# Performance work log

Measured on AMD Instinct MI355X. Metric: run time of the kernel, lower is better.

## Reference

```python
import jax, jax.numpy as jnp
import numpy as np

B, I, H = 8192, 1024, 1024

def setup_inputs() -> dict:
    key = jax.random.key(0)
    ks = jax.random.split(key, 5)
    return {
        "x": jax.random.normal(ks[0], (B, I), dtype=jnp.float32),
        "m_prev": jax.random.normal(ks[1], (B, H), dtype=jnp.float32),
        "c_prev": jax.random.normal(ks[2], (B, H), dtype=jnp.float32),
        "w_m": jax.random.normal(ks[3], (H, 8 * H), dtype=jnp.float32),
        "w_inputs": jax.random.normal(ks[4], (I, 8 * H), dtype=jnp.float32),
    }

def reference(x, m_prev, c_prev, w_m, w_inputs):
    hidden = w_m.shape[0]
    m_mat = m_prev @ w_m              # [B, 8H]
    in_mat = x @ w_inputs             # [B, 8H]
    # 8-way split along feature dim
    ms = jnp.split(m_mat, 8, axis=1)
    xs = jnp.split(in_mat, 8, axis=1)
    sig, th, rl = jax.nn.sigmoid, jnp.tanh, jax.nn.relu
    l1_0 = sig(xs[0] + ms[0])
    l1_1 = rl(xs[1] + ms[1])
    l1_2 = sig(xs[2] + ms[2])
    l1_3 = rl(xs[3] * ms[3])
    l1_4 = th(xs[4] + ms[4])
    l1_5 = sig(xs[5] + ms[5])
    l1_6 = th(xs[6] + ms[6])
    l1_7 = sig(xs[7] + ms[7])
    l2_0 = th(l1_0 * l1_1)
    l2_1 = th(l1_2 + l1_3)
    l2_2 = th(l1_4 * l1_5)
    l2_3 = sig(l1_6 + l1_7)
    l2_0 = th(l2_0 + c_prev)
    new_c = l2_0 * l2_1
    l3_1 = th(l2_2 + l2_3)
    new_m = th(new_c * l3_1)
    return (new_m, new_c)
```

## Files before the change

kernel.cpp:

```cpp
#include <hip/hip_runtime.h>
#include <stdint.h>
#include <stddef.h>


typedef _Float16 half8 __attribute__((ext_vector_type(8)));
typedef float f32x4 __attribute__((ext_vector_type(4)));
typedef float float4v __attribute__((ext_vector_type(4)));
typedef unsigned int u32;
typedef u32 u32x4 __attribute__((ext_vector_type(4)));

__device__ __forceinline__ float fsig(float x) { return 1.0f / (1.0f + __expf(-x)); }
__device__ __forceinline__ float ftanh(float x) { return 2.0f * fsig(2.0f * x) - 1.0f; }
__device__ __forceinline__ u32 packh(_Float16 a, _Float16 b) {
  union { u32 u; _Float16 h[2]; } p;
  p.h[0] = a; p.h[1] = b; return p.u;
}

__device__ __forceinline__ void gload16(const void* g, void* l) {
  __builtin_amdgcn_global_load_lds(
      (const __attribute__((address_space(1))) void*)g,
      (__attribute__((address_space(3))) void*)l, 16, 0, 0);
}

__global__ __launch_bounds__(256) void prep_b(
    const float* __restrict__ w_inputs, const float* __restrict__ w_m,
    u32* __restrict__ wsB) {
  const int kt = blockIdx.x;
  const int hblk = blockIdx.y;
  const int tid = threadIdx.x;
  const int n = tid & 15;
  const int g = (tid >> 4) & 7;
  const int mat = tid >> 7;
  const float* w = mat ? w_m : w_inputs;
  const float* src = w + (size_t)kt * 32 * 8192 + (size_t)g * 1024 + hblk * 16 + n;
  const int kx4 = ((n >> 1) & 3) << 2;
  u32 hw[16], lw[16];
#pragma unroll
  for (int k2 = 0; k2 < 16; ++k2) {
    const float v0 = src[(size_t)(2 * k2) * 8192];
    const float v1 = src[(size_t)(2 * k2 + 1) * 8192];
    const _Float16 h0 = (_Float16)v0, h1 = (_Float16)v1;
    hw[k2 ^ kx4] = packh(h0, h1);
    lw[k2 ^ kx4] = packh((_Float16)(v0 - (float)h0), (_Float16)(v1 - (float)h1));
  }
  u32* dhi = wsB + ((size_t)kt * 64 + hblk) * 8192 + mat * 2048 + g * 256 + n * 16;
  u32* dlo = dhi + 4096;
#pragma unroll
  for (int t4 = 0; t4 < 4; ++t4) {
    u32x4 a = {hw[t4 * 4], hw[t4 * 4 + 1], hw[t4 * 4 + 2], hw[t4 * 4 + 3]};
    *(u32x4*)(dhi + t4 * 4) = a;
    u32x4 b = {lw[t4 * 4], lw[t4 * 4 + 1], lw[t4 * 4 + 2], lw[t4 * 4 + 3]};
    *(u32x4*)(dlo + t4 * 4) = b;
  }
}

__global__ __launch_bounds__(256) void split_a(
    const float4v* __restrict__ in, half8* __restrict__ hi, half8* __restrict__ lo) {
  const size_t idx = (size_t)blockIdx.x * 256 + threadIdx.x;
  const float4v a = in[idx * 2];
  const float4v b = in[idx * 2 + 1];
  half8 h, l;
#pragma unroll
  for (int j = 0; j < 4; ++j) {
    const float v = a[j]; const _Float16 hv = (_Float16)v;
    h[j] = hv; l[j] = (_Float16)(v - (float)hv);
  }
#pragma unroll
  for (int j = 0; j < 4; ++j) {
    const float v = b[j]; const _Float16 hv = (_Float16)v;
    h[4 + j] = hv; l[4 + j] = (_Float16)(v - (float)hv);
  }
  hi[idx] = h; lo[idx] = l;
}

__global__ __launch_bounds__(256, 2) void nascell_fast(
    const _Float16* __restrict__ xh_g, const _Float16* __restrict__ xl_g,
    const _Float16* __restrict__ mh_g, const _Float16* __restrict__ ml_g,
    const u32* __restrict__ wsB,
    const float* __restrict__ c_prev,
    float* __restrict__ out) {
  __shared__ short lds[32768];
  const int tid = threadIdx.x;
  const int wid = tid >> 6;
  const int lane = tid & 63;
  const int row0 = blockIdx.y * 256;
  const int hblk = blockIdx.x;
  const int m16 = lane & 15;
  const int q = lane >> 4;
  const int qsw = (q ^ ((m16 >> 1) & 3)) * 8;

  const size_t arow = (size_t)(row0 + wid * 64 + m16);
  const _Float16* xhb = xh_g + arow * 1024 + q * 8;
  const _Float16* xlb = xl_g + arow * 1024 + q * 8;
  const _Float16* mhb = mh_g + arow * 1024 + q * 8;
  const _Float16* mlb = ml_g + arow * 1024 + q * 8;

  const char* wsb = (const char*)wsB + (size_t)hblk * 32768 + wid * 8192 + lane * 16;
  char* ldsb0 = (char*)lds + wid * 8192;

  f32x4 acc[4][9];
#pragma unroll
  for (int r = 0; r < 4; ++r)
#pragma unroll
    for (int gg = 0; gg < 9; ++gg) acc[r][gg] = (f32x4)0.0f;

#pragma unroll
  for (int i = 0; i < 8; ++i) gload16(wsb + i * 1024, ldsb0 + i * 1024);

  for (int kt = 0; kt < 32; ++kt) {
    __syncthreads();

    half8 axh[4], axl[4], amh[4], aml[4];
#pragma unroll
    for (int r = 0; r < 4; ++r) {
      axh[r] = *(const half8*)(xhb + (size_t)r * 16384 + kt * 32);
      axl[r] = *(const half8*)(xlb + (size_t)r * 16384 + kt * 32);
      amh[r] = *(const half8*)(mhb + (size_t)r * 16384 + kt * 32);
      aml[r] = *(const half8*)(mlb + (size_t)r * 16384 + kt * 32);
    }
    __builtin_amdgcn_sched_barrier(0);
    if (kt < 31) {
      const char* src = wsb + (size_t)(kt + 1) * 2097152;
      char* dst = (char*)lds + ((kt + 1) & 1) * 32768 + wid * 8192;
#pragma unroll
      for (int i = 0; i < 8; ++i) gload16(src + i * 1024, dst + i * 1024);
    }
    __builtin_amdgcn_sched_barrier(0);

    const short* bb = lds + (kt & 1) * 16384;

#pragma unroll
    for (int c = 0; c < 8; ++c) {
      const int bo = c * 512 + m16 * 32 + qsw;
      const half8 bxh = *(const half8*)(bb + bo);
      const half8 bxl = *(const half8*)(bb + 8192 + bo);
#pragma unroll
      for (int r = 0; r < 4; ++r) {
        f32x4 t = acc[r][c];
        t = __builtin_amdgcn_mfma_f32_16x16x32_f16(axh[r], bxh, t, 0, 0, 0);
        t = __builtin_amdgcn_mfma_f32_16x16x32_f16(axh[r], bxl, t, 0, 0, 0);
        t = __builtin_amdgcn_mfma_f32_16x16x32_f16(axl[r], bxh, t, 0, 0, 0);
        acc[r][c] = t;
      }
    }

#pragma unroll
    for (int c = 0; c < 8; ++c) {
      const int bo = 4096 + c * 512 + m16 * 32 + qsw;
      const half8 bmh = *(const half8*)(bb + bo);
      const half8 bml = *(const half8*)(bb + 8192 + bo);
      const int tgt = (c == 3) ? 8 : c;
#pragma unroll
      for (int r = 0; r < 4; ++r) {
        f32x4 t = acc[r][tgt];
        t = __builtin_amdgcn_mfma_f32_16x16x32_f16(amh[r], bmh, t, 0, 0, 0);
        t = __builtin_amdgcn_mfma_f32_16x16x32_f16(amh[r], bml, t, 0, 0, 0);
        t = __builtin_amdgcn_mfma_f32_16x16x32_f16(aml[r], bmh, t, 0, 0, 0);
        acc[r][tgt] = t;
      }
    }
  }

  float* out_m = out;
  float* out_c = out + (size_t)8192 * 1024;
  const int h = hblk * 16 + m16;
#pragma unroll
  for (int r = 0; r < 4; ++r) {
#pragma unroll
    for (int i = 0; i < 4; ++i) {
      const int grow = row0 + wid * 64 + r * 16 + q * 4 + i;
      const float p0 = acc[r][0][i], p1 = acc[r][1][i], p2 = acc[r][2][i];
      const float x3 = acc[r][3][i], p4 = acc[r][4][i], p5 = acc[r][5][i];
      const float p6 = acc[r][6][i], p7 = acc[r][7][i], m3 = acc[r][8][i];
      const float cp = c_prev[(size_t)grow * 1024 + h];
      float l1_0 = fsig(p0);
      float l1_1 = fmaxf(p1, 0.0f);
      float l1_2 = fsig(p2);
      float l1_3 = fmaxf(x3 * m3, 0.0f);
      float l1_4 = ftanh(p4);
      float l1_5 = fsig(p5);
      float l1_6 = ftanh(p6);
      float l1_7 = fsig(p7);
      float l2_0 = ftanh(l1_0 * l1_1);
      float l2_1 = ftanh(l1_2 + l1_3);
      float l2_2 = ftanh(l1_4 * l1_5);
      float l2_3 = fsig(l1_6 + l1_7);
      float l2_0b = ftanh(l2_0 + cp);
      float nc = l2_0b * l2_1;
      float l3_1 = ftanh(l2_2 + l2_3);
      float nm = ftanh(nc * l3_1);
      out_m[(size_t)grow * 1024 + h] = nm;
      out_c[(size_t)grow * 1024 + h] = nc;
    }
  }
}

__global__ __launch_bounds__(256, 2) void nascell_main(
    const float* __restrict__ x,
    const float* __restrict__ m_prev,
    const float* __restrict__ c_prev,
    const float* __restrict__ w_inputs,
    const float* __restrict__ w_m,
    float* __restrict__ out) {
  __shared__ short lds[17408];
  const int tid = threadIdx.x;
  const int wid = tid >> 6;
  const int lane = tid & 63;
  const int row0 = blockIdx.y * 256;
  const int h0 = blockIdx.x * 16;
  const int m16 = lane & 15;
  const int q = lane >> 4;

  const int bmat = tid >> 7;
  const int bg = (tid >> 4) & 7;
  const int bkp = (tid & 15) * 2;
  const float* wsrc = bmat ? w_m : w_inputs;
  const float* wrow_base = wsrc + (size_t)bkp * 8192 + (size_t)bg * 1024 + (size_t)h0;
  short* bh = lds + bmat * 4352 + bg * 544 + (bkp ^ ((bg & 3) << 3));
  short* bl = bh + 8704;

  const float* axp[4];
  const float* amp[4];
#pragma unroll
  for (int r = 0; r < 4; ++r) {
    const size_t arow = (size_t)(row0 + wid * 64 + r * 16 + m16);
    axp[r] = x + arow * 1024 + q * 8;
    amp[r] = m_prev + arow * 1024 + q * 8;
  }

  f32x4 acc[4][9];
#pragma unroll
  for (int r = 0; r < 4; ++r)
#pragma unroll
    for (int gg = 0; gg < 9; ++gg) acc[r][gg] = (f32x4)0.0f;

  for (int kt = 0; kt < 32; ++kt) {
    const float* wr = wrow_base + (size_t)kt * 32 * 8192;
    float4v b0 = *(const float4v*)(wr);
    float4v b1 = *(const float4v*)(wr + 4);
    float4v b2 = *(const float4v*)(wr + 8);
    float4v b3 = *(const float4v*)(wr + 12);
    float4v d0 = *(const float4v*)(wr + 8192);
    float4v d1 = *(const float4v*)(wr + 8196);
    float4v d2 = *(const float4v*)(wr + 8200);
    float4v d3 = *(const float4v*)(wr + 8204);

    float4v xa[4][2];
#pragma unroll
    for (int r = 0; r < 4; ++r) {
      xa[r][0] = *(const float4v*)(axp[r] + kt * 32);
      xa[r][1] = *(const float4v*)(axp[r] + kt * 32 + 4);
    }

    __syncthreads();

#pragma unroll
    for (int n = 0; n < 16; ++n) {
      const float r0 = (n < 4 ? b0[n & 3] : n < 8 ? b1[n & 3] : n < 12 ? b2[n & 3] : b3[n & 3]);
      const float r1 = (n < 4 ? d0[n & 3] : n < 8 ? d1[n & 3] : n < 12 ? d2[n & 3] : d3[n & 3]);
      const _Float16 h0v = (_Float16)r0;
      const _Float16 h1v = (_Float16)r1;
      *(u32*)(bh + n * 32) = packh(h0v, h1v);
      const _Float16 l0v = (_Float16)(r0 - (float)h0v);
      const _Float16 l1v = (_Float16)(r1 - (float)h1v);
      *(u32*)(bl + n * 32) = packh(l0v, l1v);
    }

    half8 axh[4], axl[4];
#pragma unroll
    for (int r = 0; r < 4; ++r)
#pragma unroll
      for (int j = 0; j < 8; ++j) {
        const float v = xa[r][j >> 2][j & 3];
        const _Float16 hv = (_Float16)v;
        axh[r][j] = hv;
        axl[r][j] = (_Float16)(v - (float)hv);
      }

    __syncthreads();

    float4v ma[4][2];
#pragma unroll
    for (int r = 0; r < 4; ++r) {
      ma[r][0] = *(const float4v*)(amp[r] + kt * 32);
      ma[r][1] = *(const float4v*)(amp[r] + kt * 32 + 4);
    }

#pragma unroll
    for (int c = 0; c < 8; ++c) {
      const int qs = (q ^ (c & 3)) * 8;
      const int bo = c * 544 + m16 * 32 + qs;
      half8 bxh = *(const half8*)(lds + bo);
      half8 bxl = *(const half8*)(lds + 8704 + bo);
#pragma unroll
      for (int r = 0; r < 4; ++r) {
        f32x4 t = acc[r][c];
        t = __builtin_amdgcn_mfma_f32_16x16x32_f16(axh[r], bxh, t, 0, 0, 0);
        t = __builtin_amdgcn_mfma_f32_16x16x32_f16(axh[r], bxl, t, 0, 0, 0);
        t = __builtin_amdgcn_mfma_f32_16x16x32_f16(axl[r], bxh, t, 0, 0, 0);
        acc[r][c] = t;
      }
    }

    half8 amh[4], aml[4];
#pragma unroll
    for (int r = 0; r < 4; ++r)
#pragma unroll
      for (int j = 0; j < 8; ++j) {
        const float v = ma[r][j >> 2][j & 3];
        const _Float16 hv = (_Float16)v;
        amh[r][j] = hv;
        aml[r][j] = (_Float16)(v - (float)hv);
      }

#pragma unroll
    for (int c = 0; c < 8; ++c) {
      const int qs = (q ^ (c & 3)) * 8;
      const int bo = 4352 + c * 544 + m16 * 32 + qs;
      half8 bmh = *(const half8*)(lds + bo);
      half8 bml = *(const half8*)(lds + 8704 + bo);
      const int tgt = (c == 3) ? 8 : c;
#pragma unroll
      for (int r = 0; r < 4; ++r) {
        f32x4 t = acc[r][tgt];
        t = __builtin_amdgcn_mfma_f32_16x16x32_f16(amh[r], bmh, t, 0, 0, 0);
        t = __builtin_amdgcn_mfma_f32_16x16x32_f16(amh[r], bml, t, 0, 0, 0);
        t = __builtin_amdgcn_mfma_f32_16x16x32_f16(aml[r], bmh, t, 0, 0, 0);
        acc[r][tgt] = t;
      }
    }
  }

  float* out_m = out;
  float* out_c = out + (size_t)8192 * 1024;
  const int h = h0 + m16;
#pragma unroll
  for (int r = 0; r < 4; ++r) {
#pragma unroll
    for (int i = 0; i < 4; ++i) {
      const int grow = row0 + wid * 64 + r * 16 + q * 4 + i;
      const float p0 = acc[r][0][i], p1 = acc[r][1][i], p2 = acc[r][2][i];
      const float x3 = acc[r][3][i], p4 = acc[r][4][i], p5 = acc[r][5][i];
      const float p6 = acc[r][6][i], p7 = acc[r][7][i], m3 = acc[r][8][i];
      const float cp = c_prev[(size_t)grow * 1024 + h];
      float l1_0 = fsig(p0);
      float l1_1 = fmaxf(p1, 0.0f);
      float l1_2 = fsig(p2);
      float l1_3 = fmaxf(x3 * m3, 0.0f);
      float l1_4 = ftanh(p4);
      float l1_5 = fsig(p5);
      float l1_6 = ftanh(p6);
      float l1_7 = fsig(p7);
      float l2_0 = ftanh(l1_0 * l1_1);
      float l2_1 = ftanh(l1_2 + l1_3);
      float l2_2 = ftanh(l1_4 * l1_5);
      float l2_3 = fsig(l1_6 + l1_7);
      float l2_0b = ftanh(l2_0 + cp);
      float nc = l2_0b * l2_1;
      float l3_1 = ftanh(l2_2 + l2_3);
      float nm = ftanh(nc * l3_1);
      out_m[(size_t)grow * 1024 + h] = nm;
      out_c[(size_t)grow * 1024 + h] = nc;
    }
  }
}

extern "C" void kernel_launch(void* const* d_in, const int* in_sizes, int n_in,
                              void* d_out, int out_size, void* d_ws, size_t ws_size,
                              hipStream_t stream) {
  (void)in_sizes; (void)n_in; (void)out_size;
  const float* x        = (const float*)d_in[0];
  const float* m_prev   = (const float*)d_in[1];
  const float* c_prev   = (const float*)d_in[2];
  const float* w_m      = (const float*)d_in[3];
  const float* w_inputs = (const float*)d_in[4];
  float* out = (float*)d_out;

  if (ws_size >= 134217728ull && d_ws != nullptr) {
    u32* wsB = (u32*)d_ws;
    _Float16* xh = (_Float16*)((char*)d_ws + 67108864);
    _Float16* xl = xh + 8388608;
    _Float16* mh = xl + 8388608;
    _Float16* ml = mh + 8388608;
    prep_b<<<dim3(32, 64), 256, 0, stream>>>(w_inputs, w_m, wsB);
    split_a<<<4096, 256, 0, stream>>>((const float4v*)x, (half8*)xh, (half8*)xl);
    split_a<<<4096, 256, 0, stream>>>((const float4v*)m_prev, (half8*)mh, (half8*)ml);
    nascell_fast<<<dim3(64, 32), 256, 0, stream>>>(xh, xl, mh, ml, wsB, c_prev, out);
  } else {
    dim3 grid(64, 32);
    nascell_main<<<grid, 256, 0, stream>>>(x, m_prev, c_prev, w_inputs, w_m, out);
  }
}
```

Baseline: 873.0 us.

## Read B fragments directly from global in MFMA layout, drop LDS staging

The weight prep kernel now writes hi/lo fp16 tiles laid out so each lane can load its MFMA B fragment with one contiguous 16-byte global load. The main kernel drops the LDS double buffer, global_load_lds prefetch and per-iteration __syncthreads, and reads B straight from global/L2. The two activation split launches are merged into one launch. This removes barrier and LDS traffic but loses the explicit prefetch overlap, and all four waves in a block now read the same B tile from cache.

```diff
diff --git a/kernel.cpp b/kernel.cpp
--- a/kernel.cpp
+++ b/kernel.cpp
@@ -16,15 +16,9 @@
   p.h[0] = a; p.h[1] = b; return p.u;
 }
 
-__device__ __forceinline__ void gload16(const void* g, void* l) {
-  __builtin_amdgcn_global_load_lds(
-      (const __attribute__((address_space(1))) void*)g,
-      (__attribute__((address_space(3))) void*)l, 16, 0, 0);
-}
-
 __global__ __launch_bounds__(256) void prep_b(
     const float* __restrict__ w_inputs, const float* __restrict__ w_m,
-    u32* __restrict__ wsB) {
+    char* __restrict__ wsB) {
   const int kt = blockIdx.x;
   const int hblk = blockIdx.y;
   const int tid = threadIdx.x;
@@ -33,29 +27,36 @@
   const int mat = tid >> 7;
   const float* w = mat ? w_m : w_inputs;
   const float* src = w + (size_t)kt * 32 * 8192 + (size_t)g * 1024 + hblk * 16 + n;
-  const int kx4 = ((n >> 1) & 3) << 2;
-  u32 hw[16], lw[16];
-#pragma unroll
-  for (int k2 = 0; k2 < 16; ++k2) {
-    const float v0 = src[(size_t)(2 * k2) * 8192];
-    const float v1 = src[(size_t)(2 * k2 + 1) * 8192];
-    const _Float16 h0 = (_Float16)v0, h1 = (_Float16)v1;
-    hw[k2 ^ kx4] = packh(h0, h1);
-    lw[k2 ^ kx4] = packh((_Float16)(v0 - (float)h0), (_Float16)(v1 - (float)h1));
-  }
-  u32* dhi = wsB + ((size_t)kt * 64 + hblk) * 8192 + mat * 2048 + g * 256 + n * 16;
-  u32* dlo = dhi + 4096;
-#pragma unroll
-  for (int t4 = 0; t4 < 4; ++t4) {
-    u32x4 a = {hw[t4 * 4], hw[t4 * 4 + 1], hw[t4 * 4 + 2], hw[t4 * 4 + 3]};
-    *(u32x4*)(dhi + t4 * 4) = a;
-    u32x4 b = {lw[t4 * 4], lw[t4 * 4 + 1], lw[t4 * 4 + 2], lw[t4 * 4 + 3]};
-    *(u32x4*)(dlo + t4 * 4) = b;
-  }
-}
-
-__global__ __launch_bounds__(256) void split_a(
-    const float4v* __restrict__ in, half8* __restrict__ hi, half8* __restrict__ lo) {
+  _Float16 hs[32], ls[32];
+#pragma unroll
+  for (int k = 0; k < 32; ++k) {
+    const float v = src[(size_t)k * 8192];
+    const _Float16 h = (_Float16)v;
+    hs[k] = h;
+    ls[k] = (_Float16)(v - (float)h);
+  }
+  char* tile = wsB + ((size_t)hblk * 32 + kt) * 32768;
+  char* hi = tile + (size_t)((mat * 8 + g) * 2 + 0) * 1024;
+  char* lo = hi + 1024;
+#pragma unroll
+  for (int kc = 0; kc < 4; ++kc) {
+    u32x4 a = {packh(hs[kc * 8 + 0], hs[kc * 8 + 1]), packh(hs[kc * 8 + 2], hs[kc * 8 + 3]),
+               packh(hs[kc * 8 + 4], hs[kc * 8 + 5]), packh(hs[kc * 8 + 6], hs[kc * 8 + 7])};
+    *(u32x4*)(hi + (kc * 16 + n) * 16) = a;
+    u32x4 b = {packh(ls[kc * 8 + 0], ls[kc * 8 + 1]), packh(ls[kc * 8 + 2], ls[kc * 8 + 3]),
+               packh(ls[kc * 8 + 4], ls[kc * 8 + 5]), packh(ls[kc * 8 + 6], ls[kc * 8 + 7])};
+    *(u32x4*)(lo + (kc * 16 + n) * 16) = b;
+  }
+}
+
+__global__ __launch_bounds__(256) void split_ab(
+    const float4v* __restrict__ xin, const float4v* __restrict__ min,
+    half8* __restrict__ xhi, half8* __restrict__ xlo,
+    half8* __restrict__ mhi, half8* __restrict__ mlo) {
+  const int which = blockIdx.y;
+  const float4v* in = which ? min : xin;
+  half8* hi = which ? mhi : xhi;
+  half8* lo = which ? mlo : xlo;
   const size_t idx = (size_t)blockIdx.x * 256 + threadIdx.x;
   const float4v a = in[idx * 2];
   const float4v b = in[idx * 2 + 1];
@@ -73,13 +74,12 @@
   hi[idx] = h; lo[idx] = l;
 }
 
-__global__ __launch_bounds__(256, 2) void nascell_fast(
+__global__ __launch_bounds__(256, 2) void nascell_v3(
     const _Float16* __restrict__ xh_g, const _Float16* __restrict__ xl_g,
     const _Float16* __restrict__ mh_g, const _Float16* __restrict__ ml_g,
-    const u32* __restrict__ wsB,
+    const char* __restrict__ wsB,
     const float* __restrict__ c_prev,
     float* __restrict__ out) {
-  __shared__ short lds[32768];
   const int tid = threadIdx.x;
   const int wid = tid >> 6;
   const int lane = tid & 63;
@@ -87,7 +87,6 @@
   const int hblk = blockIdx.x;
   const int m16 = lane & 15;
   const int q = lane >> 4;
-  const int qsw = (q ^ ((m16 >> 1) & 3)) * 8;
 
   const size_t arow = (size_t)(row0 + wid * 64 + m16);
   const _Float16* xhb = xh_g + arow * 1024 + q * 8;
@@ -95,8 +94,7 @@
   const _Float16* mhb = mh_g + arow * 1024 + q * 8;
   const _Float16* mlb = ml_g + arow * 1024 + q * 8;
 
-  const char* wsb = (const char*)wsB + (size_t)hblk * 32768 + wid * 8192 + lane * 16;
-  char* ldsb0 = (char*)lds + wid * 8192;
+  const char* bt = wsB + (size_t)hblk * 32 * 32768 + lane * 16;
 
   f32x4 acc[4][9];
 #pragma unroll
@@ -104,11 +102,9 @@
 #pragma unroll
     for (int gg = 0; gg < 9; ++gg) acc[r][gg] = (f32x4)0.0f;
 
-#pragma unroll
-  for (int i = 0; i < 8; ++i) gload16(wsb + i * 1024, ldsb0 + i * 1024);
-
+#pragma unroll 1
   for (int kt = 0; kt < 32; ++kt) {
-    __syncthreads();
+    const char* tb = bt + (size_t)kt * 32768;
 
     half8 axh[4], axl[4], amh[4], aml[4];
 #pragma unroll
@@ -118,22 +114,11 @@
       amh[r] = *(const half8*)(mhb + (size_t)r * 16384 + kt * 32);
       aml[r] = *(const half8*)(mlb + (size_t)r * 16384 + kt * 32);
     }
-    __builtin_amdgcn_sched_barrier(0);
-    if (kt < 31) {
-      const char* src = wsb + (size_t)(kt + 1) * 2097152;
-      char* dst = (char*)lds + ((kt + 1) & 1) * 32768 + wid * 8192;
-#pragma unroll
-      for (int i = 0; i < 8; ++i) gload16(src + i * 1024, dst + i * 1024);
-    }
-    __builtin_amdgcn_sched_barrier(0);
-
-    const short* bb = lds + (kt & 1) * 16384;
 
 #pragma unroll
     for (int c = 0; c < 8; ++c) {
-      const int bo = c * 512 + m16 * 32 + qsw;
-      const half8 bxh = *(const half8*)(bb + bo);
-      const half8 bxl = *(const half8*)(bb + 8192 + bo);
+      const half8 bxh = *(const half8*)(tb + (size_t)(c * 2) * 1024);
+      const half8 bxl = *(const half8*)(tb + (size_t)(c * 2 + 1) * 1024);
 #pragma unroll
       for (int r = 0; r < 4; ++r) {
         f32x4 t = acc[r][c];
@@ -146,9 +131,8 @@
 
 #pragma unroll
     for (int c = 0; c < 8; ++c) {
-      const int bo = 4096 + c * 512 + m16 * 32 + qsw;
-      const half8 bmh = *(const half8*)(bb + bo);
-      const half8 bml = *(const half8*)(bb + 8192 + bo);
+      const half8 bmh = *(const half8*)(tb + 16384 + (size_t)(c * 2) * 1024);
+      const half8 bml = *(const half8*)(tb + 16384 + (size_t)(c * 2 + 1) * 1024);
       const int tgt = (c == 3) ? 8 : c;
 #pragma unroll
       for (int r = 0; r < 4; ++r) {
@@ -377,15 +361,16 @@
   float* out = (float*)d_out;
 
   if (ws_size >= 134217728ull && d_ws != nullptr) {
-    u32* wsB = (u32*)d_ws;
+    char* wsB = (char*)d_ws;
     _Float16* xh = (_Float16*)((char*)d_ws + 67108864);
     _Float16* xl = xh + 8388608;
     _Float16* mh = xl + 8388608;
     _Float16* ml = mh + 8388608;
     prep_b<<<dim3(32, 64), 256, 0, stream>>>(w_inputs, w_m, wsB);
-    split_a<<<4096, 256, 0, stream>>>((const float4v*)x, (half8*)xh, (half8*)xl);
-    split_a<<<4096, 256, 0, stream>>>((const float4v*)m_prev, (half8*)mh, (half8*)ml);
-    nascell_fast<<<dim3(64, 32), 256, 0, stream>>>(xh, xl, mh, ml, wsB, c_prev, out);
+    split_ab<<<dim3(4096, 2), 256, 0, stream>>>(
+        (const float4v*)x, (const float4v*)m_prev,
+        (half8*)xh, (half8*)xl, (half8*)mh, (half8*)ml);
+    nascell_v3<<<dim3(64, 32), 256, 0, stream>>>(xh, xl, mh, ml, wsB, c_prev, out);
   } else {
     dim3 grid(64, 32);
     nascell_main<<<grid, 256, 0, stream>>>(x, m_prev, c_prev, w_inputs, w_m, out);
```

Measured after the change: 1.053 ms. 20.6% more time.

## Merge prep kernels and deepen GEMM pipeline to four LDS stages

Applied to the files above, without the earlier changes.

Merges the weight-repacking and activation-splitting kernels into one launch and moves the weight workspace to an hblk-major layout so each block reads contiguous chunks. The main GEMM loop now splits each k-tile into separate x and m half-stages across four 16KB LDS slots. It waits on explicit vmcnt counts with raw s_barrier instead of __syncthreads, and uses setprio around the MFMA passes. The goal is to keep more loads in flight and overlap global-to-LDS copies with MFMA work, at the cost of fragile hand-managed waitcnt accounting.

```diff
diff --git a/kernel.cpp b/kernel.cpp
--- a/kernel.cpp
+++ b/kernel.cpp
@@ -22,64 +22,146 @@
       (__attribute__((address_space(3))) void*)l, 16, 0, 0);
 }
 
-__global__ __launch_bounds__(256) void prep_b(
+__global__ __launch_bounds__(256) void prep_all(
     const float* __restrict__ w_inputs, const float* __restrict__ w_m,
-    u32* __restrict__ wsB) {
-  const int kt = blockIdx.x;
-  const int hblk = blockIdx.y;
+    const float4v* __restrict__ xin, const float4v* __restrict__ min,
+    u32* __restrict__ wsB,
+    half8* __restrict__ xhi, half8* __restrict__ xlo,
+    half8* __restrict__ mhi, half8* __restrict__ mlo) {
+  const int bid = blockIdx.x;
   const int tid = threadIdx.x;
-  const int n = tid & 15;
-  const int g = (tid >> 4) & 7;
-  const int mat = tid >> 7;
-  const float* w = mat ? w_m : w_inputs;
-  const float* src = w + (size_t)kt * 32 * 8192 + (size_t)g * 1024 + hblk * 16 + n;
-  const int kx4 = ((n >> 1) & 3) << 2;
-  u32 hw[16], lw[16];
-#pragma unroll
-  for (int k2 = 0; k2 < 16; ++k2) {
-    const float v0 = src[(size_t)(2 * k2) * 8192];
-    const float v1 = src[(size_t)(2 * k2 + 1) * 8192];
-    const _Float16 h0 = (_Float16)v0, h1 = (_Float16)v1;
-    hw[k2 ^ kx4] = packh(h0, h1);
-    lw[k2 ^ kx4] = packh((_Float16)(v0 - (float)h0), (_Float16)(v1 - (float)h1));
-  }
-  u32* dhi = wsB + ((size_t)kt * 64 + hblk) * 8192 + mat * 2048 + g * 256 + n * 16;
-  u32* dlo = dhi + 4096;
-#pragma unroll
-  for (int t4 = 0; t4 < 4; ++t4) {
-    u32x4 a = {hw[t4 * 4], hw[t4 * 4 + 1], hw[t4 * 4 + 2], hw[t4 * 4 + 3]};
-    *(u32x4*)(dhi + t4 * 4) = a;
-    u32x4 b = {lw[t4 * 4], lw[t4 * 4 + 1], lw[t4 * 4 + 2], lw[t4 * 4 + 3]};
-    *(u32x4*)(dlo + t4 * 4) = b;
-  }
-}
-
-__global__ __launch_bounds__(256) void split_a(
-    const float4v* __restrict__ in, half8* __restrict__ hi, half8* __restrict__ lo) {
-  const size_t idx = (size_t)blockIdx.x * 256 + threadIdx.x;
-  const float4v a = in[idx * 2];
-  const float4v b = in[idx * 2 + 1];
-  half8 h, l;
-#pragma unroll
-  for (int j = 0; j < 4; ++j) {
-    const float v = a[j]; const _Float16 hv = (_Float16)v;
-    h[j] = hv; l[j] = (_Float16)(v - (float)hv);
-  }
-#pragma unroll
-  for (int j = 0; j < 4; ++j) {
-    const float v = b[j]; const _Float16 hv = (_Float16)v;
-    h[4 + j] = hv; l[4 + j] = (_Float16)(v - (float)hv);
-  }
-  hi[idx] = h; lo[idx] = l;
-}
-
-__global__ __launch_bounds__(256, 2) void nascell_fast(
+  if (bid < 2048) {
+    const int kt = bid & 31;
+    const int hblk = bid >> 5;
+    const int n = tid & 15;
+    const int g = (tid >> 4) & 7;
+    const int mat = tid >> 7;
+    const float* w = mat ? w_m : w_inputs;
+    const float* src = w + (size_t)kt * 32 * 8192 + (size_t)g * 1024 + hblk * 16 + n;
+    const int kx4 = ((n >> 1) & 3) << 2;
+    u32 hw[16], lw[16];
+#pragma unroll
+    for (int k2 = 0; k2 < 16; ++k2) {
+      const float v0 = src[(size_t)(2 * k2) * 8192];
+      const float v1 = src[(size_t)(2 * k2 + 1) * 8192];
+      const _Float16 h0 = (_Float16)v0, h1 = (_Float16)v1;
+      hw[k2 ^ kx4] = packh(h0, h1);
+      lw[k2 ^ kx4] = packh((_Float16)(v0 - (float)h0), (_Float16)(v1 - (float)h1));
+    }
+    u32* dhi = wsB + ((size_t)(hblk * 32 + kt) * 2 + mat) * 4096 + g * 256 + n * 16;
+    u32* dlo = dhi + 2048;
+#pragma unroll
+    for (int t4 = 0; t4 < 4; ++t4) {
+      u32x4 a = {hw[t4 * 4], hw[t4 * 4 + 1], hw[t4 * 4 + 2], hw[t4 * 4 + 3]};
+      *(u32x4*)(dhi + t4 * 4) = a;
+      u32x4 b = {lw[t4 * 4], lw[t4 * 4 + 1], lw[t4 * 4 + 2], lw[t4 * 4 + 3]};
+      *(u32x4*)(dlo + t4 * 4) = b;
+    }
+  } else {
+    const int sid = bid - 2048;
+    const int which = sid >> 12;
+    const int bx = sid & 4095;
+    const float4v* in = which ? min : xin;
+    half8* hi = which ? mhi : xhi;
+    half8* lo = which ? mlo : xlo;
+    const size_t idx = (size_t)bx * 256 + tid;
+    const float4v a = in[idx * 2];
+    const float4v b = in[idx * 2 + 1];
+    half8 h, l;
+#pragma unroll
+    for (int j = 0; j < 4; ++j) {
+      const float v = a[j]; const _Float16 hv = (_Float16)v;
+      h[j] = hv; l[j] = (_Float16)(v - (float)hv);
+    }
+#pragma unroll
+    for (int j = 0; j < 4; ++j) {
+      const float v = b[j]; const _Float16 hv = (_Float16)v;
+      h[4 + j] = hv; l[4 + j] = (_Float16)(v - (float)hv);
+    }
+    hi[idx] = h; lo[idx] = l;
+  }
+}
+
+
+#define NAS_WAITBAR(Wlit)                                                  \
+  do {                                                                     \
+    asm volatile("s_waitcnt vmcnt(" #Wlit ")" ::: "memory");               \
+    __builtin_amdgcn_s_barrier();                                          \
+    __builtin_amdgcn_sched_barrier(0);                                     \
+  } while (0)
+
+#define NAS_STAGE(KT, MAT, SLOT)                                           \
+  do {                                                                     \
+    const char* s_ = wsb + (size_t)(((KT) * 2 + (MAT)) * 16384);           \
+    char* d_ = ldsb + (SLOT) * 16384;                                      \
+    gload16(s_, d_);                                                       \
+    gload16(s_ + 4096, d_ + 4096);                                         \
+    gload16(s_ + 8192, d_ + 8192);                                         \
+    gload16(s_ + 12288, d_ + 12288);                                       \
+  } while (0)
+
+#define NAS_LOADX(KT)                                                      \
+  do {                                                                     \
+    _Pragma("unroll") for (int r_ = 0; r_ < 4; ++r_) {                     \
+      axh[r_] = *(const half8*)(xhb + r_ * 16384 + (KT) * 32);             \
+      axl[r_] = *(const half8*)(xlb + r_ * 16384 + (KT) * 32);             \
+    }                                                                      \
+  } while (0)
+
+#define NAS_LOADM(KT)                                                      \
+  do {                                                                     \
+    _Pragma("unroll") for (int r_ = 0; r_ < 4; ++r_) {                     \
+      amh[r_] = *(const half8*)(mhb + r_ * 16384 + (KT) * 32);             \
+      aml[r_] = *(const half8*)(mlb + r_ * 16384 + (KT) * 32);             \
+    }                                                                      \
+  } while (0)
+
+#define NAS_XPASS(SLOT)                                                    \
+  do {                                                                     \
+    const short* bb_ = lds_s + (SLOT) * 8192;                              \
+    __builtin_amdgcn_s_setprio(1);                                         \
+    _Pragma("unroll") for (int c_ = 0; c_ < 8; ++c_) {                     \
+      const int bo_ = c_ * 512 + m16 * 32 + qsw;                           \
+      const half8 bh_ = *(const half8*)(bb_ + bo_);                        \
+      const half8 bl_ = *(const half8*)(bb_ + 4096 + bo_);                 \
+      _Pragma("unroll") for (int r_ = 0; r_ < 4; ++r_) {                   \
+        f32x4 t_ = acc[r_][c_];                                            \
+        t_ = __builtin_amdgcn_mfma_f32_16x16x32_f16(axh[r_], bh_, t_, 0, 0, 0); \
+        t_ = __builtin_amdgcn_mfma_f32_16x16x32_f16(axh[r_], bl_, t_, 0, 0, 0); \
+        t_ = __builtin_amdgcn_mfma_f32_16x16x32_f16(axl[r_], bh_, t_, 0, 0, 0); \
+        acc[r_][c_] = t_;                                                  \
+      }                                                                    \
+    }                                                                      \
+    __builtin_amdgcn_s_setprio(0);                                         \
+  } while (0)
+
+#define NAS_MPASS(SLOT)                                                    \
+  do {                                                                     \
+    const short* bb_ = lds_s + (SLOT) * 8192;                              \
+    __builtin_amdgcn_s_setprio(1);                                         \
+    _Pragma("unroll") for (int c_ = 0; c_ < 8; ++c_) {                     \
+      const int bo_ = c_ * 512 + m16 * 32 + qsw;                           \
+      const half8 bh_ = *(const half8*)(bb_ + bo_);                        \
+      const half8 bl_ = *(const half8*)(bb_ + 4096 + bo_);                 \
+      const int tgt_ = (c_ == 3) ? 8 : c_;                                 \
+      _Pragma("unroll") for (int r_ = 0; r_ < 4; ++r_) {                   \
+        f32x4 t_ = acc[r_][tgt_];                                          \
+        t_ = __builtin_amdgcn_mfma_f32_16x16x32_f16(amh[r_], bh_, t_, 0, 0, 0); \
+        t_ = __builtin_amdgcn_mfma_f32_16x16x32_f16(amh[r_], bl_, t_, 0, 0, 0); \
+        t_ = __builtin_amdgcn_mfma_f32_16x16x32_f16(aml[r_], bh_, t_, 0, 0, 0); \
+        acc[r_][tgt_] = t_;                                                \
+      }                                                                    \
+    }                                                                      \
+    __builtin_amdgcn_s_setprio(0);                                         \
+  } while (0)
+
+__global__ __launch_bounds__(256, 2) void nascell_v6(
     const _Float16* __restrict__ xh_g, const _Float16* __restrict__ xl_g,
     const _Float16* __restrict__ mh_g, const _Float16* __restrict__ ml_g,
-    const u32* __restrict__ wsB,
+    const char* __restrict__ wsB,
     const float* __restrict__ c_prev,
     float* __restrict__ out) {
-  __shared__ short lds[32768];
+  __shared__ short lds_s[32768];
   const int tid = threadIdx.x;
   const int wid = tid >> 6;
   const int lane = tid & 63;
@@ -89,14 +171,13 @@
   const int q = lane >> 4;
   const int qsw = (q ^ ((m16 >> 1) & 3)) * 8;
 
-  const size_t arow = (size_t)(row0 + wid * 64 + m16);
-  const _Float16* xhb = xh_g + arow * 1024 + q * 8;
-  const _Float16* xlb = xl_g + arow * 1024 + q * 8;
-  const _Float16* mhb = mh_g + arow * 1024 + q * 8;
-  const _Float16* mlb = ml_g + arow * 1024 + q * 8;
-
-  const char* wsb = (const char*)wsB + (size_t)hblk * 32768 + wid * 8192 + lane * 16;
-  char* ldsb0 = (char*)lds + wid * 8192;
+  const _Float16* xhb = xh_g + (size_t)(row0 + wid * 64 + m16) * 1024 + q * 8;
+  const _Float16* xlb = xl_g + (size_t)(row0 + wid * 64 + m16) * 1024 + q * 8;
+  const _Float16* mhb = mh_g + (size_t)(row0 + wid * 64 + m16) * 1024 + q * 8;
+  const _Float16* mlb = ml_g + (size_t)(row0 + wid * 64 + m16) * 1024 + q * 8;
+
+  const char* wsb = wsB + (size_t)hblk * 1048576 + tid * 16;
+  char* ldsb = (char*)lds_s + tid * 16;
 
   f32x4 acc[4][9];
 #pragma unroll
@@ -104,62 +185,26 @@
 #pragma unroll
     for (int gg = 0; gg < 9; ++gg) acc[r][gg] = (f32x4)0.0f;
 
-#pragma unroll
-  for (int i = 0; i < 8; ++i) gload16(wsb + i * 1024, ldsb0 + i * 1024);
-
-  for (int kt = 0; kt < 32; ++kt) {
-    __syncthreads();
-
-    half8 axh[4], axl[4], amh[4], aml[4];
-#pragma unroll
-    for (int r = 0; r < 4; ++r) {
-      axh[r] = *(const half8*)(xhb + (size_t)r * 16384 + kt * 32);
-      axl[r] = *(const half8*)(xlb + (size_t)r * 16384 + kt * 32);
-      amh[r] = *(const half8*)(mhb + (size_t)r * 16384 + kt * 32);
-      aml[r] = *(const half8*)(mlb + (size_t)r * 16384 + kt * 32);
-    }
-    __builtin_amdgcn_sched_barrier(0);
-    if (kt < 31) {
-      const char* src = wsb + (size_t)(kt + 1) * 2097152;
-      char* dst = (char*)lds + ((kt + 1) & 1) * 32768 + wid * 8192;
-#pragma unroll
-      for (int i = 0; i < 8; ++i) gload16(src + i * 1024, dst + i * 1024);
-    }
-    __builtin_amdgcn_sched_barrier(0);
-
-    const short* bb = lds + (kt & 1) * 16384;
-
-#pragma unroll
-    for (int c = 0; c < 8; ++c) {
-      const int bo = c * 512 + m16 * 32 + qsw;
-      const half8 bxh = *(const half8*)(bb + bo);
-      const half8 bxl = *(const half8*)(bb + 8192 + bo);
-#pragma unroll
-      for (int r = 0; r < 4; ++r) {
-        f32x4 t = acc[r][c];
-        t = __builtin_amdgcn_mfma_f32_16x16x32_f16(axh[r], bxh, t, 0, 0, 0);
-        t = __builtin_amdgcn_mfma_f32_16x16x32_f16(axh[r], bxl, t, 0, 0, 0);
-        t = __builtin_amdgcn_mfma_f32_16x16x32_f16(axl[r], bxh, t, 0, 0, 0);
-        acc[r][c] = t;
-      }
-    }
-
-#pragma unroll
-    for (int c = 0; c < 8; ++c) {
-      const int bo = 4096 + c * 512 + m16 * 32 + qsw;
-      const half8 bmh = *(const half8*)(bb + bo);
-      const half8 bml = *(const half8*)(bb + 8192 + bo);
-      const int tgt = (c == 3) ? 8 : c;
-#pragma unroll
-      for (int r = 0; r < 4; ++r) {
-        f32x4 t = acc[r][tgt];
-        t = __builtin_amdgcn_mfma_f32_16x16x32_f16(amh[r], bmh, t, 0, 0, 0);
-        t = __builtin_amdgcn_mfma_f32_16x16x32_f16(amh[r], bml, t, 0, 0, 0);
-        t = __builtin_amdgcn_mfma_f32_16x16x32_f16(aml[r], bmh, t, 0, 0, 0);
-        acc[r][tgt] = t;
-      }
-    }
-  }
+  half8 axh[4], axl[4], amh[4], aml[4];
+
+  NAS_STAGE(0, 0, 0);
+  NAS_STAGE(0, 1, 1);
+  NAS_STAGE(1, 0, 2);
+  NAS_LOADX(0);
+
+#pragma unroll 1
+  for (int ktp = 0; ktp < 15; ++ktp) {
+    const int kt0 = 2 * ktp, kt1 = 2 * ktp + 1;
+    const int kt2 = 2 * ktp + 2, kt3 = 2 * ktp + 3;
+    NAS_WAITBAR(16); NAS_LOADM(kt0); NAS_STAGE(kt1, 1, 3); NAS_XPASS(0);
+    NAS_WAITBAR(16); NAS_LOADX(kt1); NAS_STAGE(kt2, 0, 0); NAS_MPASS(1);
+    NAS_WAITBAR(16); NAS_LOADM(kt1); NAS_STAGE(kt2, 1, 1); NAS_XPASS(2);
+    NAS_WAITBAR(16); NAS_LOADX(kt2); NAS_STAGE(kt3, 0, 2); NAS_MPASS(3);
+  }
+  NAS_WAITBAR(16); NAS_LOADM(30); NAS_STAGE(31, 1, 3); NAS_XPASS(0);
+  NAS_WAITBAR(16); NAS_LOADX(31); NAS_MPASS(1);
+  NAS_WAITBAR(12); NAS_LOADM(31); NAS_XPASS(2);
+  NAS_WAITBAR(8);  NAS_MPASS(3);
 
   float* out_m = out;
   float* out_c = out + (size_t)8192 * 1024;
@@ -382,10 +427,11 @@
     _Float16* xl = xh + 8388608;
     _Float16* mh = xl + 8388608;
     _Float16* ml = mh + 8388608;
-    prep_b<<<dim3(32, 64), 256, 0, stream>>>(w_inputs, w_m, wsB);
-    split_a<<<4096, 256, 0, stream>>>((const float4v*)x, (half8*)xh, (half8*)xl);
-    split_a<<<4096, 256, 0, stream>>>((const float4v*)m_prev, (half8*)mh, (half8*)ml);
-    nascell_fast<<<dim3(64, 32), 256, 0, stream>>>(xh, xl, mh, ml, wsB, c_prev, out);
+    prep_all<<<10240, 256, 0, stream>>>(
+        w_inputs, w_m, (const float4v*)x, (const float4v*)m_prev, wsB,
+        (half8*)xh, (half8*)xl, (half8*)mh, (half8*)ml);
+    nascell_v6<<<dim3(64, 32), 256, 0, stream>>>(
+        xh, xl, mh, ml, (const char*)d_ws, c_prev, out);
   } else {
     dim3 grid(64, 32);
     nascell_main<<<grid, 256, 0, stream>>>(x, m_prev, c_prev, w_inputs, w_m, out);
```

New measurement: 1.184 ms. +35.6%, slower.
